# Kernel tuning notes

Measured on AMD Instinct MI355X. Metric: run time of the kernel, lower is better.

## Reference

```python
import jax, jax.numpy as jnp
import numpy as np

WL = 8          # windowlen
LOSS_TH = 10.0  # losss threshold
BIT = 8


def _round(x):
    return jnp.round(x)


def part_quant1(x, mx, bitwidth, en=1):
    if en == 1:
        lsb = 2.0 ** (_round(jnp.log2(mx / 2.0 ** (bitwidth - 1))) + 1.0)
    else:
        lsb = 2.0 ** (_round(jnp.log2(mx / 2.0 ** bitwidth)) + 1.0)
    return _round(x / lsb) * lsb


def setup_inputs() -> dict:
    key = jax.random.key(0)
    x = jax.random.normal(key, (1, 16, 1024, 1024), dtype=jnp.float32)
    return {"x": x}


def reference(x):
    B, N, H, W = x.shape  # B must be 1
    wl = WL
    Wb, Hb = W // wl, H // wl

    # delta_comp: column-wise delta with zero pad on the left
    x_left = jnp.pad(x[..., : W - 1], ((0, 0), (0, 0), (0, 0), (1, 0)))
    xc = x - x_left

    In_max = jnp.abs(xc).max()
    x1 = part_quant1(xc, In_max, BIT, en=1)

    # blockify: d has shape (Wb, Hb, wl*wl, N); d1 is (Wb, Hb, N, wl*wl)
    b = x1.reshape(B, N, H, Wb, wl).transpose(0, 1, 3, 2, 4)           # B,N,Wb,H,wl
    c = b.reshape(B, N, Wb, Hb, wl, wl).transpose(0, 2, 3, 1, 4, 5)    # B,Wb,Hb,N,wl,wl
    d = c.reshape(B, Wb, Hb, N, wl * wl).transpose(0, 1, 2, 4, 3)[0]   # Wb,Hb,wl^2,N
    d1 = jnp.swapaxes(d, -1, -2)                                       # Wb,Hb,N,wl^2

    a1 = d1[:, :, 0:1, :]
    a2 = d1[:, :, 1:2, :]
    a3 = jnp.ones_like(a1)
    a_base = jnp.concatenate([a1, a2, a3], axis=2)                     # Wb,Hb,3,wl^2

    # blocks where both basis images are (near) constant
    flat = ((a1.max(-1) - a1.min(-1)).squeeze(-1) < 1e-6) & \
           ((a2.max(-1) - a2.min(-1)).squeeze(-1) < 1e-6)              # Wb,Hb

    ATA = jnp.einsum('whik,whjk->whij', a_base, a_base)                # Wb,Hb,3,3
    det = jnp.linalg.det(ATA)
    eye3 = jnp.eye(3, dtype=x.dtype)
    ATA = jnp.where((det == 0)[..., None, None], eye3, ATA)
    ATA_inv = jnp.linalg.inv(ATA)

    base = ATA_inv @ a_base                                            # Wb,Hb,3,wl^2
    p = base @ d                                                       # Wb,Hb,3,N
    r = jnp.swapaxes(a_base, -1, -2) @ p                               # Wb,Hb,wl^2,N
    r1 = part_quant1(jnp.swapaxes(r, -1, -2), In_max, BIT, en=1)       # Wb,Hb,N,wl^2

    loss_sum = ((d1 - r1) ** 2).sum(-1)                                # Wb,Hb,N
    rr = jnp.where((loss_sum <= LOSS_TH)[..., None], r1, d1)
    rr = jnp.where(flat[:, :, None, None], d1, rr)

    # deblockify back to (1, N, H, W)
    rr = rr.reshape(Wb, Hb, N, wl, wl).transpose(2, 1, 3, 0, 4).reshape(N, H, W)[None]

    # delta_dcom
    return rr + x_left
```

## Files before the change

### kernel.cpp

```cpp
#include <hip/hip_runtime.h>

static constexpr int Hh  = 1024;
static constexpr int Wd  = 1024;
static constexpr int NCH = 16;

__global__ __launch_bounds__(256) void k_maxabs(const float* __restrict__ x,
                                                unsigned int* __restrict__ omax,
                                                int n4) {
    float m = 0.0f;
    int stride = gridDim.x * blockDim.x;
    for (int i = blockIdx.x * blockDim.x + threadIdx.x; i < n4; i += stride) {
        float4 v = reinterpret_cast<const float4*>(x)[i];
        int w0 = (i * 4) & (Wd - 1);
        float left = (w0 == 0) ? 0.0f : x[i * 4 - 1];
        float d0 = v.x - left;
        float d1 = v.y - v.x;
        float d2 = v.z - v.y;
        float d3 = v.w - v.z;
        m = fmaxf(m, fmaxf(fmaxf(fabsf(d0), fabsf(d1)), fmaxf(fabsf(d2), fabsf(d3))));
    }
#pragma unroll
    for (int off = 32; off >= 1; off >>= 1)
        m = fmaxf(m, __shfl_xor(m, off));
    __shared__ float smax[4];
    int lane = threadIdx.x & 63;
    int wv   = threadIdx.x >> 6;
    if (lane == 0) smax[wv] = m;
    __syncthreads();
    if (threadIdx.x == 0) {
        float mm = fmaxf(fmaxf(smax[0], smax[1]), fmaxf(smax[2], smax[3]));
        atomicMax(omax, __float_as_uint(mm));
    }
}

__device__ __forceinline__ float quantv(float v, float inv_lsb, float lsb) {
    return rintf(v * inv_lsb) * lsb;
}

__global__ __launch_bounds__(256) void k_blocks(const float* __restrict__ x,
                                                const unsigned int* __restrict__ pmax,
                                                float* __restrict__ out) {
    const int blk = blockIdx.x;
    const int wb  = blk & 127;
    const int hb  = blk >> 7;
    const int w0  = wb * 8;
    const int h0  = hb * 8;
    const int tid = threadIdx.x;

    __shared__ float raw[128][12];

    for (int v = tid; v < 384; v += 256) {
        int row = v / 3;
        int seg = v - row * 3;
        int n = row >> 3, i = row & 7;
        float4 val;
        if (seg == 0 && wb == 0) {
            val = make_float4(0.f, 0.f, 0.f, 0.f);
        } else {
            int gidx = (n * Hh + (h0 + i)) * Wd + (w0 - 4 + seg * 4);
            val = *reinterpret_cast<const float4*>(x + gidx);
        }
        *reinterpret_cast<float4*>(&raw[row][seg * 4]) = val;
    }
    __syncthreads();

    const float mx      = __uint_as_float(*pmax);
    const float lsb     = exp2f(rintf(log2f(mx * 0.0078125f)) + 1.0f);
    const float inv_lsb = 1.0f / lsb;

    const int n  = tid >> 4;
    const int g  = tid & 15;
    const int ri = g >> 1;
    const int jb = (g & 1) * 4;

    const float* rown = raw[n * 8 + ri];
    const float* row0 = raw[0 * 8 + ri];
    const float* row1 = raw[1 * 8 + ri];

    float xl[4], dv[4], a1v[4], a2v[4];
#pragma unroll
    for (int q = 0; q < 4; ++q) {
        int c  = 3 + jb + q;
        xl[q]  = rown[c];
        dv[q]  = quantv(rown[c + 1] - rown[c], inv_lsb, lsb);
        a1v[q] = quantv(row0[c + 1] - row0[c], inv_lsb, lsb);
        a2v[q] = quantv(row1[c + 1] - row1[c], inv_lsb, lsb);
    }

    float s11 = 0.f, s12 = 0.f, s22 = 0.f, s1 = 0.f, s2 = 0.f;
    float mn1 = a1v[0], mx1 = a1v[0], mn2 = a2v[0], mx2 = a2v[0];
#pragma unroll
    for (int q = 0; q < 4; ++q) {
        s11 += a1v[q] * a1v[q];
        s12 += a1v[q] * a2v[q];
        s22 += a2v[q] * a2v[q];
        s1  += a1v[q];
        s2  += a2v[q];
        mn1 = fminf(mn1, a1v[q]); mx1 = fmaxf(mx1, a1v[q]);
        mn2 = fminf(mn2, a2v[q]); mx2 = fmaxf(mx2, a2v[q]);
    }
#pragma unroll
    for (int off = 1; off < 16; off <<= 1) {
        s11 += __shfl_xor(s11, off);
        s12 += __shfl_xor(s12, off);
        s22 += __shfl_xor(s22, off);
        s1  += __shfl_xor(s1,  off);
        s2  += __shfl_xor(s2,  off);
        mn1 = fminf(mn1, __shfl_xor(mn1, off));
        mx1 = fmaxf(mx1, __shfl_xor(mx1, off));
        mn2 = fminf(mn2, __shfl_xor(mn2, off));
        mx2 = fmaxf(mx2, __shfl_xor(mx2, off));
    }
    const bool flat = ((mx1 - mn1) < 1e-6f) && ((mx2 - mn2) < 1e-6f);

    const float a00 = s11, a01 = s12, a02 = s1;
    const float a10 = s12, a11 = s22, a12 = s2;
    const float a20 = s1,  a21 = s2,  a22 = 64.0f;
    const float det = a00 * a11 * a22 + a01 * a12 * a20 + a02 * a10 * a21
                    - a02 * a11 * a20 - a00 * a12 * a21 - a01 * a10 * a22;

    float i00, i01, i02, i11, i12, i22;
    if (det == 0.0f) {
        i00 = 1.f; i01 = 0.f; i02 = 0.f; i11 = 1.f; i12 = 0.f; i22 = 1.f;
    } else {
        const float rd = 1.0f / det;
        i00 = (a11 * a22 - a12 * a21) * rd;
        i01 = (a02 * a21 - a01 * a22) * rd;
        i02 = (a01 * a12 - a02 * a11) * rd;
        i11 = (a00 * a22 - a02 * a20) * rd;
        i12 = (a02 * a10 - a00 * a12) * rd;
        i22 = (a00 * a11 - a01 * a10) * rd;
    }

    float m0 = 0.f, m1 = 0.f, m2 = 0.f;
#pragma unroll
    for (int q = 0; q < 4; ++q) {
        m0 += a1v[q] * dv[q];
        m1 += a2v[q] * dv[q];
        m2 += dv[q];
    }
#pragma unroll
    for (int off = 1; off < 16; off <<= 1) {
        m0 += __shfl_xor(m0, off);
        m1 += __shfl_xor(m1, off);
        m2 += __shfl_xor(m2, off);
    }
    const float p0 = i00 * m0 + i01 * m1 + i02 * m2;
    const float p1 = i01 * m0 + i11 * m1 + i12 * m2;
    const float p2 = i02 * m0 + i12 * m1 + i22 * m2;

    float r1v[4];
    float loss = 0.f;
#pragma unroll
    for (int q = 0; q < 4; ++q) {
        float r  = a1v[q] * p0 + a2v[q] * p1 + p2;
        r1v[q]   = quantv(r, inv_lsb, lsb);
        float df = dv[q] - r1v[q];
        loss += df * df;
    }
#pragma unroll
    for (int off = 1; off < 16; off <<= 1)
        loss += __shfl_xor(loss, off);

    const bool use_r = (!flat) && (loss <= 10.0f);

    float4 o;
    o.x = (use_r ? r1v[0] : dv[0]) + xl[0];
    o.y = (use_r ? r1v[1] : dv[1]) + xl[1];
    o.z = (use_r ? r1v[2] : dv[2]) + xl[2];
    o.w = (use_r ? r1v[3] : dv[3]) + xl[3];

    const int oidx = (n * Hh + (h0 + ri)) * Wd + w0 + jb;
    *reinterpret_cast<float4*>(out + oidx) = o;
}

extern "C" void kernel_launch(void* const* d_in, const int* in_sizes, int n_in,
                              void* d_out, int out_size, void* d_ws, size_t ws_size,
                              hipStream_t stream) {
    const float* x = (const float*)d_in[0];
    float* out     = (float*)d_out;
    unsigned int* pmax = (unsigned int*)d_ws;

    hipMemsetAsync(d_ws, 0, sizeof(unsigned int), stream);

    const int n4 = (NCH * Hh * Wd) / 4;
    k_maxabs<<<2048, 256, 0, stream>>>(x, pmax, n4);

    k_blocks<<<128 * 128, 256, 0, stream>>>(x, pmax, out);
}
```

Measured before the change: 197.3 us.

## Process 8 blocks per workgroup with transposed LDS tile and XCD-aware block mapping

Each workgroup in k_blocks now loads a 64-column strip for all 16 channels and 8 rows into a transposed, padded LDS tile. It then loops over 8 horizontal 8x8 blocks, which cuts the redundant left-halo loads and the launch of 16K tiny workgroups down to 2K larger ones. The block index is remapped so that consecutive tiles land on the same XCD for L2 locality. k_maxabs takes its left neighbour from a wave shuffle instead of a second global load. The transposed LDS writes may cause bank conflicts, and the new sequential per-block loop lowers parallelism per workgroup.

```diff
diff --git a/kernel.cpp b/kernel.cpp
--- a/kernel.cpp
+++ b/kernel.cpp
@@ -8,11 +8,20 @@
                                                 unsigned int* __restrict__ omax,
                                                 int n4) {
     float m = 0.0f;
-    int stride = gridDim.x * blockDim.x;
+    const int stride = gridDim.x * blockDim.x;
+    const int lane = threadIdx.x & 63;
     for (int i = blockIdx.x * blockDim.x + threadIdx.x; i < n4; i += stride) {
         float4 v = reinterpret_cast<const float4*>(x)[i];
+        float prevw = __shfl_up(v.w, 1);
         int w0 = (i * 4) & (Wd - 1);
-        float left = (w0 == 0) ? 0.0f : x[i * 4 - 1];
+        float left;
+        if (w0 == 0) {
+            left = 0.0f;
+        } else if (lane == 0) {
+            left = x[i * 4 - 1];
+        } else {
+            left = prevw;
+        }
         float d0 = v.x - left;
         float d1 = v.y - v.x;
         float d2 = v.z - v.y;
@@ -23,8 +32,7 @@
     for (int off = 32; off >= 1; off >>= 1)
         m = fmaxf(m, __shfl_xor(m, off));
     __shared__ float smax[4];
-    int lane = threadIdx.x & 63;
-    int wv   = threadIdx.x >> 6;
+    int wv = threadIdx.x >> 6;
     if (lane == 0) smax[wv] = m;
     __syncthreads();
     if (threadIdx.x == 0) {
@@ -40,27 +48,42 @@
 __global__ __launch_bounds__(256) void k_blocks(const float* __restrict__ x,
                                                 const unsigned int* __restrict__ pmax,
                                                 float* __restrict__ out) {
-    const int blk = blockIdx.x;
-    const int wb  = blk & 127;
-    const int hb  = blk >> 7;
-    const int w0  = wb * 8;
-    const int h0  = hb * 8;
+    const int bid = blockIdx.x;
+    const int xcd = bid & 7;
+    const int lin = xcd * 256 + (bid >> 3);
+    const int hb  = lin >> 4;
+    const int wg  = lin & 15;
+    const int w_base = wg * 64;
+    const int h0     = hb * 8;
     const int tid = threadIdx.x;
 
-    __shared__ float raw[128][12];
-
-    for (int v = tid; v < 384; v += 256) {
-        int row = v / 3;
-        int seg = v - row * 3;
-        int n = row >> 3, i = row & 7;
+    __shared__ float lds[68][129];
+
+    for (int v = tid; v < 2048; v += 256) {
+        const int row = v >> 4;
+        const int j   = v & 15;
+        const int ch  = row >> 3, r = row & 7;
+        const int gidx = (ch * Hh + (h0 + r)) * Wd + w_base + j * 4;
+        float4 val = *reinterpret_cast<const float4*>(x + gidx);
+        lds[4 + j * 4 + 0][row] = val.x;
+        lds[4 + j * 4 + 1][row] = val.y;
+        lds[4 + j * 4 + 2][row] = val.z;
+        lds[4 + j * 4 + 3][row] = val.w;
+    }
+    if (tid < 128) {
+        const int row = tid;
+        const int ch = row >> 3, r = row & 7;
         float4 val;
-        if (seg == 0 && wb == 0) {
+        if (wg == 0) {
             val = make_float4(0.f, 0.f, 0.f, 0.f);
         } else {
-            int gidx = (n * Hh + (h0 + i)) * Wd + (w0 - 4 + seg * 4);
+            const int gidx = (ch * Hh + (h0 + r)) * Wd + w_base - 4;
             val = *reinterpret_cast<const float4*>(x + gidx);
         }
-        *reinterpret_cast<float4*>(&raw[row][seg * 4]) = val;
+        lds[0][row] = val.x;
+        lds[1][row] = val.y;
+        lds[2][row] = val.z;
+        lds[3][row] = val.w;
     }
     __syncthreads();
 
@@ -68,110 +91,114 @@
     const float lsb     = exp2f(rintf(log2f(mx * 0.0078125f)) + 1.0f);
     const float inv_lsb = 1.0f / lsb;
 
-    const int n  = tid >> 4;
+    const int ch = tid >> 4;
     const int g  = tid & 15;
     const int ri = g >> 1;
     const int jb = (g & 1) * 4;
 
-    const float* rown = raw[n * 8 + ri];
-    const float* row0 = raw[0 * 8 + ri];
-    const float* row1 = raw[1 * 8 + ri];
-
-    float xl[4], dv[4], a1v[4], a2v[4];
-#pragma unroll
-    for (int q = 0; q < 4; ++q) {
-        int c  = 3 + jb + q;
-        xl[q]  = rown[c];
-        dv[q]  = quantv(rown[c + 1] - rown[c], inv_lsb, lsb);
-        a1v[q] = quantv(row0[c + 1] - row0[c], inv_lsb, lsb);
-        a2v[q] = quantv(row1[c + 1] - row1[c], inv_lsb, lsb);
-    }
-
-    float s11 = 0.f, s12 = 0.f, s22 = 0.f, s1 = 0.f, s2 = 0.f;
-    float mn1 = a1v[0], mx1 = a1v[0], mn2 = a2v[0], mx2 = a2v[0];
-#pragma unroll
-    for (int q = 0; q < 4; ++q) {
-        s11 += a1v[q] * a1v[q];
-        s12 += a1v[q] * a2v[q];
-        s22 += a2v[q] * a2v[q];
-        s1  += a1v[q];
-        s2  += a2v[q];
-        mn1 = fminf(mn1, a1v[q]); mx1 = fmaxf(mx1, a1v[q]);
-        mn2 = fminf(mn2, a2v[q]); mx2 = fmaxf(mx2, a2v[q]);
-    }
-#pragma unroll
-    for (int off = 1; off < 16; off <<= 1) {
-        s11 += __shfl_xor(s11, off);
-        s12 += __shfl_xor(s12, off);
-        s22 += __shfl_xor(s22, off);
-        s1  += __shfl_xor(s1,  off);
-        s2  += __shfl_xor(s2,  off);
-        mn1 = fminf(mn1, __shfl_xor(mn1, off));
-        mx1 = fmaxf(mx1, __shfl_xor(mx1, off));
-        mn2 = fminf(mn2, __shfl_xor(mn2, off));
-        mx2 = fmaxf(mx2, __shfl_xor(mx2, off));
-    }
-    const bool flat = ((mx1 - mn1) < 1e-6f) && ((mx2 - mn2) < 1e-6f);
-
-    const float a00 = s11, a01 = s12, a02 = s1;
-    const float a10 = s12, a11 = s22, a12 = s2;
-    const float a20 = s1,  a21 = s2,  a22 = 64.0f;
-    const float det = a00 * a11 * a22 + a01 * a12 * a20 + a02 * a10 * a21
-                    - a02 * a11 * a20 - a00 * a12 * a21 - a01 * a10 * a22;
-
-    float i00, i01, i02, i11, i12, i22;
-    if (det == 0.0f) {
-        i00 = 1.f; i01 = 0.f; i02 = 0.f; i11 = 1.f; i12 = 0.f; i22 = 1.f;
-    } else {
-        const float rd = 1.0f / det;
-        i00 = (a11 * a22 - a12 * a21) * rd;
-        i01 = (a02 * a21 - a01 * a22) * rd;
-        i02 = (a01 * a12 - a02 * a11) * rd;
-        i11 = (a00 * a22 - a02 * a20) * rd;
-        i12 = (a02 * a10 - a00 * a12) * rd;
-        i22 = (a00 * a11 - a01 * a10) * rd;
-    }
-
-    float m0 = 0.f, m1 = 0.f, m2 = 0.f;
-#pragma unroll
-    for (int q = 0; q < 4; ++q) {
-        m0 += a1v[q] * dv[q];
-        m1 += a2v[q] * dv[q];
-        m2 += dv[q];
-    }
-#pragma unroll
-    for (int off = 1; off < 16; off <<= 1) {
-        m0 += __shfl_xor(m0, off);
-        m1 += __shfl_xor(m1, off);
-        m2 += __shfl_xor(m2, off);
-    }
-    const float p0 = i00 * m0 + i01 * m1 + i02 * m2;
-    const float p1 = i01 * m0 + i11 * m1 + i12 * m2;
-    const float p2 = i02 * m0 + i12 * m1 + i22 * m2;
-
-    float r1v[4];
-    float loss = 0.f;
-#pragma unroll
-    for (int q = 0; q < 4; ++q) {
-        float r  = a1v[q] * p0 + a2v[q] * p1 + p2;
-        r1v[q]   = quantv(r, inv_lsb, lsb);
-        float df = dv[q] - r1v[q];
-        loss += df * df;
-    }
-#pragma unroll
-    for (int off = 1; off < 16; off <<= 1)
-        loss += __shfl_xor(loss, off);
-
-    const bool use_r = (!flat) && (loss <= 10.0f);
-
-    float4 o;
-    o.x = (use_r ? r1v[0] : dv[0]) + xl[0];
-    o.y = (use_r ? r1v[1] : dv[1]) + xl[1];
-    o.z = (use_r ? r1v[2] : dv[2]) + xl[2];
-    o.w = (use_r ? r1v[3] : dv[3]) + xl[3];
-
-    const int oidx = (n * Hh + (h0 + ri)) * Wd + w0 + jb;
-    *reinterpret_cast<float4*>(out + oidx) = o;
+    const int rowN = ch * 8 + ri;
+    const int r0   = ri;
+    const int r1   = 8 + ri;
+
+    for (int sb = 0; sb < 8; ++sb) {
+        const int cb = 4 + sb * 8 + jb;
+
+        float xl[4], dvv[4], a1v[4], a2v[4];
+#pragma unroll
+        for (int q = 0; q < 4; ++q) {
+            const int c = cb + q;
+            xl[q]  = lds[c - 1][rowN];
+            dvv[q] = quantv(lds[c][rowN] - xl[q], inv_lsb, lsb);
+            a1v[q] = quantv(lds[c][r0] - lds[c - 1][r0], inv_lsb, lsb);
+            a2v[q] = quantv(lds[c][r1] - lds[c - 1][r1], inv_lsb, lsb);
+        }
+
+        float s11 = 0.f, s12 = 0.f, s22 = 0.f, s1 = 0.f, s2 = 0.f;
+        float mn1 = a1v[0], mx1 = a1v[0], mn2 = a2v[0], mx2 = a2v[0];
+#pragma unroll
+        for (int q = 0; q < 4; ++q) {
+            s11 += a1v[q] * a1v[q];
+            s12 += a1v[q] * a2v[q];
+            s22 += a2v[q] * a2v[q];
+            s1  += a1v[q];
+            s2  += a2v[q];
+            mn1 = fminf(mn1, a1v[q]); mx1 = fmaxf(mx1, a1v[q]);
+            mn2 = fminf(mn2, a2v[q]); mx2 = fmaxf(mx2, a2v[q]);
+        }
+#pragma unroll
+        for (int off = 1; off < 16; off <<= 1) {
+            s11 += __shfl_xor(s11, off);
+            s12 += __shfl_xor(s12, off);
+            s22 += __shfl_xor(s22, off);
+            s1  += __shfl_xor(s1,  off);
+            s2  += __shfl_xor(s2,  off);
+            mn1 = fminf(mn1, __shfl_xor(mn1, off));
+            mx1 = fmaxf(mx1, __shfl_xor(mx1, off));
+            mn2 = fminf(mn2, __shfl_xor(mn2, off));
+            mx2 = fmaxf(mx2, __shfl_xor(mx2, off));
+        }
+        const bool flat = ((mx1 - mn1) < 1e-6f) && ((mx2 - mn2) < 1e-6f);
+
+        const float a00 = s11, a01 = s12, a02 = s1;
+        const float a10 = s12, a11 = s22, a12 = s2;
+        const float a20 = s1,  a21 = s2,  a22 = 64.0f;
+        const float det = a00 * a11 * a22 + a01 * a12 * a20 + a02 * a10 * a21
+                        - a02 * a11 * a20 - a00 * a12 * a21 - a01 * a10 * a22;
+
+        float i00, i01, i02, i11, i12, i22;
+        if (det == 0.0f) {
+            i00 = 1.f; i01 = 0.f; i02 = 0.f; i11 = 1.f; i12 = 0.f; i22 = 1.f;
+        } else {
+            const float rd = 1.0f / det;
+            i00 = (a11 * a22 - a12 * a21) * rd;
+            i01 = (a02 * a21 - a01 * a22) * rd;
+            i02 = (a01 * a12 - a02 * a11) * rd;
+            i11 = (a00 * a22 - a02 * a20) * rd;
+            i12 = (a02 * a10 - a00 * a12) * rd;
+            i22 = (a00 * a11 - a01 * a10) * rd;
+        }
+
+        float m0 = 0.f, m1 = 0.f, m2 = 0.f;
+#pragma unroll
+        for (int q = 0; q < 4; ++q) {
+            m0 += a1v[q] * dvv[q];
+            m1 += a2v[q] * dvv[q];
+            m2 += dvv[q];
+        }
+#pragma unroll
+        for (int off = 1; off < 16; off <<= 1) {
+            m0 += __shfl_xor(m0, off);
+            m1 += __shfl_xor(m1, off);
+            m2 += __shfl_xor(m2, off);
+        }
+        const float p0 = i00 * m0 + i01 * m1 + i02 * m2;
+        const float p1 = i01 * m0 + i11 * m1 + i12 * m2;
+        const float p2 = i02 * m0 + i12 * m1 + i22 * m2;
+
+        float r1v[4];
+        float loss = 0.f;
+#pragma unroll
+        for (int q = 0; q < 4; ++q) {
+            float r  = a1v[q] * p0 + a2v[q] * p1 + p2;
+            r1v[q]   = quantv(r, inv_lsb, lsb);
+            float df = dvv[q] - r1v[q];
+            loss += df * df;
+        }
+#pragma unroll
+        for (int off = 1; off < 16; off <<= 1)
+            loss += __shfl_xor(loss, off);
+
+        const bool use_r = (!flat) && (loss <= 10.0f);
+
+        float4 o;
+        o.x = (use_r ? r1v[0] : dvv[0]) + xl[0];
+        o.y = (use_r ? r1v[1] : dvv[1]) + xl[1];
+        o.z = (use_r ? r1v[2] : dvv[2]) + xl[2];
+        o.w = (use_r ? r1v[3] : dvv[3]) + xl[3];
+
+        const int oidx = (ch * Hh + (h0 + ri)) * Wd + w_base + sb * 8 + jb;
+        *reinterpret_cast<float4*>(out + oidx) = o;
+    }
 }
 
 extern "C" void kernel_launch(void* const* d_in, const int* in_sizes, int n_in,
@@ -186,5 +213,5 @@
     const int n4 = (NCH * Hh * Wd) / 4;
     k_maxabs<<<2048, 256, 0, stream>>>(x, pmax, n4);
 
-    k_blocks<<<128 * 128, 256, 0, stream>>>(x, pmax, out);
-}
+    k_blocks<<<128 * 16, 256, 0, stream>>>(x, pmax, out);
+}
```

Result: faster. 172.3 us (-12.7%).
